# Kernel optimization log

Hardware: AMD Instinct MI355X
Metric: run time of the kernel (lower is better)

The kernel has to match this reference:

```python
import jax, jax.numpy as jnp
import numpy as np


def _mixture_log_cdf(x, pi, mu, s):
    # x: (B, C, H, W); pi/mu/s: (B, K, C, H, W); logistic log-CDF = log_sigmoid(z)
    z = (x[:, None] - mu) * jnp.exp(-s)
    return jax.scipy.special.logsumexp(
        jax.nn.log_softmax(pi, axis=1) + jax.nn.log_sigmoid(z), axis=1)


def _mixture_log_pdf(x, pi, mu, s):
    # logistic log-pdf: -z - log_scale - 2*softplus(-z), z = (x - mu) / exp(s)
    z = (x[:, None] - mu) * jnp.exp(-s)
    log_pdf = -z - s - 2.0 * jax.nn.softplus(-z)
    return jax.scipy.special.logsumexp(
        jax.nn.log_softmax(pi, axis=1) + log_pdf, axis=1)


def setup_inputs() -> dict:
    key = jax.random.key(0)
    B, C, H, W, K = 16, 64, 64, 64, 16
    Ch = C // 2
    ks = jax.random.split(key, 6)
    return {
        'x': jax.random.normal(ks[0], (B, C, H, W), jnp.float32),
        'sldj': jnp.zeros((B,), jnp.float32),
        'a': jax.random.normal(ks[1], (B, Ch, H, W), jnp.float32),
        'b': jax.random.normal(ks[2], (B, Ch, H, W), jnp.float32),
        'pi': jax.random.normal(ks[3], (B, K, Ch, H, W), jnp.float32),
        'mu': jax.random.normal(ks[4], (B, K, Ch, H, W), jnp.float32),
        's': jax.random.normal(ks[5], (B, K, Ch, H, W), jnp.float32),
    }


def reference(x, sldj, a, b, pi, mu, s):
    C = x.shape[1]
    x_change, x_id = x[:, :C // 2], x[:, C // 2:]
    # forward direction (reverse=False)
    log_cdf = _mixture_log_cdf(x_change, pi, mu, s)   # (B, C/2, H, W)
    u = jnp.exp(log_cdf)
    # logistic.inverse: logit(u); ldj = -log(u) - log(1-u)
    out = jnp.log(u) - jnp.log1p(-u)
    scale_ldj = -jnp.log(u) - jnp.log1p(-u)
    out = (out + b) * jnp.exp(a)
    logistic_ldj = _mixture_log_pdf(x_change, pi, mu, s)
    sldj = sldj + (logistic_ldj + scale_ldj + a).reshape(x.shape[0], -1).sum(-1)
    return jnp.concatenate([out, x_id], axis=1), sldj
```

## Files before the change

kernel.cpp:

```cpp
#include <hip/hip_runtime.h>
#include <math.h>

typedef float f32x4 __attribute__((ext_vector_type(4)));

constexpr int NB = 16, NK = 16, NCh = 32, NH = 64, NW = 64;
constexpr int HW = NH * NW;
constexpr int PER_BATCH = NCh * HW;
constexpr int NTOT = NB * PER_BATCH;
constexpr int PMS_BSTRIDE = NK * PER_BATCH;
constexpr int TILE = 1024;
constexpr int NTILES = NTOT / TILE;
constexpr int NBLOCKS = 1024;
constexpr int TPB = NTILES / NBLOCKS;

#define GLOAD4(dst, addr) \
    asm volatile("global_load_dwordx4 %0, %1, off" : "=v"(dst) : "v"(addr))

#define VMWAIT(N)                                              \
    do {                                                       \
        asm volatile("s_waitcnt vmcnt(" #N ")" ::: "memory");  \
        __builtin_amdgcn_sched_barrier(0);                     \
    } while (0)

#define ISSUE(buf, kbase)                                                     \
    do {                                                                      \
        _Pragma("unroll") for (int j = 0; j < 4; ++j) {                       \
            GLOAD4(Pb[buf][j], pp + (size_t)((kbase) + j) * PER_BATCH);       \
            GLOAD4(Mb[buf][j], mp + (size_t)((kbase) + j) * PER_BATCH);       \
            GLOAD4(Sb[buf][j], sp + (size_t)((kbase) + j) * PER_BATCH);       \
        }                                                                     \
    } while (0)

#define COMPUTE(buf)                                                          \
    do {                                                                      \
        _Pragma("unroll") for (int j = 0; j < 4; ++j) {                       \
            _Pragma("unroll") for (int e = 0; e < 4; ++e) {                   \
                const float es = __expf(-Sb[buf][j][e]);                      \
                float z = (x4[e] - Mb[buf][j][e]) * es;                       \
                z = fmaxf(z, -87.0f);                \
                const float t   = __expf(-z);                                 \
                const float sig = __builtin_amdgcn_rcpf(1.0f + t);            \
                const float ep  = __expf(Pb[buf][j][e]);                      \
                const float epc = ep * sig;                                   \
                const float cc  = epc * t;                                    \
                sumw[e]  += ep;                                               \
                scdf[e]  += epc;                                              \
                sccdf[e] += cc;                                               \
                spdf[e]   = fmaf(cc, sig * es, spdf[e]);                      \
            }                                                                 \
        }                                                                     \
    } while (0)

__launch_bounds__(256)
__global__ void mixlogcdf_kernel(const float* __restrict__ x,
                                 const float* __restrict__ a,
                                 const float* __restrict__ b,
                                 const float* __restrict__ pi,
                                 const float* __restrict__ mu,
                                 const float* __restrict__ s,
                                 float* __restrict__ out,
                                 float* __restrict__ ws) {
    const int blk = blockIdx.x;
    float srow = 0.f;

    for (int t = 0; t < TPB; ++t) {
        const int tile  = blk * TPB + t;
        const int gid   = tile * TILE + (threadIdx.x << 2);
        const int batch = gid >> 17;
        const int rem   = gid & (PER_BATCH - 1);
        const int xbase = (batch << 18) | rem;

        const size_t base = (size_t)batch * PMS_BSTRIDE + rem;
        const float* pp = pi + base;
        const float* mp = mu + base;
        const float* sp = s + base;

        f32x4 x4, a4, b4, id4;
        GLOAD4(x4, x + xbase);
        GLOAD4(a4, a + gid);
        GLOAD4(b4, b + gid);
        GLOAD4(id4, x + xbase + PER_BATCH);

        f32x4 Pb[2][4], Mb[2][4], Sb[2][4];
        ISSUE(0, 0);
        ISSUE(1, 4);

        float sumw[4]  = {0.f, 0.f, 0.f, 0.f};
        float scdf[4]  = {0.f, 0.f, 0.f, 0.f};
        float sccdf[4] = {0.f, 0.f, 0.f, 0.f};
        float spdf[4]  = {0.f, 0.f, 0.f, 0.f};

        VMWAIT(12);
        COMPUTE(0);
        ISSUE(0, 8);
        VMWAIT(12);
        COMPUTE(1);
        ISSUE(1, 12);
        VMWAIT(12);
        COMPUTE(0);
        VMWAIT(0);
        COMPUTE(1);

        f32x4 o4;
#pragma unroll
        for (int e = 0; e < 4; ++e) {
            const float lsp  = __logf(sumw[e]);
            const float lsc  = __logf(fmaxf(scdf[e], 1e-37f));
            const float lscc = __logf(fmaxf(sccdf[e], 1e-37f));
            const float lst  = __logf(fmaxf(spdf[e], 1e-37f));
            o4[e] = (lsc - lscc + b4[e]) * __expf(a4[e]);
            srow += lst + lsp - lsc - lscc + a4[e];
        }
        *(f32x4*)(out + xbase) = o4;
        *(f32x4*)(out + xbase + PER_BATCH) = id4;
    }

#pragma unroll
    for (int off = 32; off > 0; off >>= 1) srow += __shfl_down(srow, off, 64);
    __shared__ float wsum[4];
    const int lane = threadIdx.x & 63;
    const int wid  = threadIdx.x >> 6;
    if (lane == 0) wsum[wid] = srow;
    __syncthreads();
    if (threadIdx.x == 0) ws[blk] = wsum[0] + wsum[1] + wsum[2] + wsum[3];
}

__global__ void sldj_reduce_kernel(const float* __restrict__ sldj_in,
                                   const float* __restrict__ ws,
                                   float* __restrict__ out_sldj) {
    const int bb = blockIdx.x;
    float v = ws[bb * 64 + threadIdx.x];
#pragma unroll
    for (int off = 32; off > 0; off >>= 1) v += __shfl_down(v, off, 64);
    if (threadIdx.x == 0) out_sldj[bb] = sldj_in[bb] + v;
}

extern "C" void kernel_launch(void* const* d_in, const int* in_sizes, int n_in,
                              void* d_out, int out_size, void* d_ws, size_t ws_size,
                              hipStream_t stream) {
    const float* x    = (const float*)d_in[0];
    const float* sldj = (const float*)d_in[1];
    const float* a    = (const float*)d_in[2];
    const float* b    = (const float*)d_in[3];
    const float* pi   = (const float*)d_in[4];
    const float* mu   = (const float*)d_in[5];
    const float* s    = (const float*)d_in[6];

    float* out      = (float*)d_out;
    float* out_sldj = out + (size_t)NB * 2 * PER_BATCH;
    float* wsf      = (float*)d_ws;

    mixlogcdf_kernel<<<NBLOCKS, 256, 0, stream>>>(x, a, b, pi, mu, s, out, wsf);
    sldj_reduce_kernel<<<NB, 64, 0, stream>>>(sldj, wsf, out_sldj);
}
```

Baseline: 88.95 us.

## Stream pi and mu through LDS via global_load_lds double buffering

```diff
diff --git a/kernel.cpp b/kernel.cpp
--- a/kernel.cpp
+++ b/kernel.cpp
@@ -22,34 +22,16 @@
         __builtin_amdgcn_sched_barrier(0);                     \
     } while (0)
 
-#define ISSUE(buf, kbase)                                                     \
-    do {                                                                      \
-        _Pragma("unroll") for (int j = 0; j < 4; ++j) {                       \
-            GLOAD4(Pb[buf][j], pp + (size_t)((kbase) + j) * PER_BATCH);       \
-            GLOAD4(Mb[buf][j], mp + (size_t)((kbase) + j) * PER_BATCH);       \
-            GLOAD4(Sb[buf][j], sp + (size_t)((kbase) + j) * PER_BATCH);       \
-        }                                                                     \
+#define LGKM0()                                                \
+    do {                                                       \
+        asm volatile("s_waitcnt lgkmcnt(0)" ::: "memory");     \
+        __builtin_amdgcn_sched_barrier(0);                     \
     } while (0)
 
-#define COMPUTE(buf)                                                          \
-    do {                                                                      \
-        _Pragma("unroll") for (int j = 0; j < 4; ++j) {                       \
-            _Pragma("unroll") for (int e = 0; e < 4; ++e) {                   \
-                const float es = __expf(-Sb[buf][j][e]);                      \
-                float z = (x4[e] - Mb[buf][j][e]) * es;                       \
-                z = fmaxf(z, -87.0f);                \
-                const float t   = __expf(-z);                                 \
-                const float sig = __builtin_amdgcn_rcpf(1.0f + t);            \
-                const float ep  = __expf(Pb[buf][j][e]);                      \
-                const float epc = ep * sig;                                   \
-                const float cc  = epc * t;                                    \
-                sumw[e]  += ep;                                               \
-                scdf[e]  += epc;                                              \
-                sccdf[e] += cc;                                               \
-                spdf[e]   = fmaf(cc, sig * es, spdf[e]);                      \
-            }                                                                 \
-        }                                                                     \
-    } while (0)
+#define DMA16(gp, ldsptr)                                                     \
+    __builtin_amdgcn_global_load_lds(                                         \
+        (const __attribute__((address_space(1))) void*)(gp),                  \
+        (__attribute__((address_space(3))) void*)(ldsptr), 16, 0, 0)
 
 __launch_bounds__(256)
 __global__ void mixlogcdf_kernel(const float* __restrict__ x,
@@ -60,6 +42,11 @@
                                  const float* __restrict__ s,
                                  float* __restrict__ out,
                                  float* __restrict__ ws) {
+    __shared__ float lds[4 * 2048];
+    const int wid   = threadIdx.x >> 6;
+    const int lane  = threadIdx.x & 63;
+    const int wbase = wid * 2048;
+
     const int blk = blockIdx.x;
     float srow = 0.f;
 
@@ -70,10 +57,12 @@
         const int rem   = gid & (PER_BATCH - 1);
         const int xbase = (batch << 18) | rem;
 
-        const size_t base = (size_t)batch * PMS_BSTRIDE + rem;
-        const float* pp = pi + base;
-        const float* mp = mu + base;
-        const float* sp = s + base;
+        const size_t tbase = (size_t)batch * PMS_BSTRIDE + rem;
+        const float* sp = s + tbase;
+        const int wrem = (tile * TILE + wid * 256) & (PER_BATCH - 1);
+        const size_t wb = (size_t)batch * PMS_BSTRIDE + wrem + lane * 4;
+        const float* pw = pi + wb;
+        const float* mw = mu + wb;
 
         f32x4 x4, a4, b4, id4;
         GLOAD4(x4, x + xbase);
@@ -81,25 +70,73 @@
         GLOAD4(b4, b + gid);
         GLOAD4(id4, x + xbase + PER_BATCH);
 
-        f32x4 Pb[2][4], Mb[2][4], Sb[2][4];
-        ISSUE(0, 0);
-        ISSUE(1, 4);
+        f32x4 Sb[2][2];
+        DMA16(pw + 0 * PER_BATCH, &lds[wbase + 0 * 1024 + 0 * 512 + 0 * 256]);
+        DMA16(pw + 1 * PER_BATCH, &lds[wbase + 0 * 1024 + 1 * 512 + 0 * 256]);
+        DMA16(mw + 0 * PER_BATCH, &lds[wbase + 0 * 1024 + 0 * 512 + 1 * 256]);
+        DMA16(mw + 1 * PER_BATCH, &lds[wbase + 0 * 1024 + 1 * 512 + 1 * 256]);
+        GLOAD4(Sb[0][0], sp + 0 * PER_BATCH);
+        GLOAD4(Sb[0][1], sp + 1 * PER_BATCH);
+        DMA16(pw + 2 * PER_BATCH, &lds[wbase + 1 * 1024 + 0 * 512 + 0 * 256]);
+        DMA16(pw + 3 * PER_BATCH, &lds[wbase + 1 * 1024 + 1 * 512 + 0 * 256]);
+        DMA16(mw + 2 * PER_BATCH, &lds[wbase + 1 * 1024 + 0 * 512 + 1 * 256]);
+        DMA16(mw + 3 * PER_BATCH, &lds[wbase + 1 * 1024 + 1 * 512 + 1 * 256]);
+        GLOAD4(Sb[1][0], sp + 2 * PER_BATCH);
+        GLOAD4(Sb[1][1], sp + 3 * PER_BATCH);
 
         float sumw[4]  = {0.f, 0.f, 0.f, 0.f};
         float scdf[4]  = {0.f, 0.f, 0.f, 0.f};
         float sccdf[4] = {0.f, 0.f, 0.f, 0.f};
         float spdf[4]  = {0.f, 0.f, 0.f, 0.f};
 
-        VMWAIT(12);
-        COMPUTE(0);
-        ISSUE(0, 8);
-        VMWAIT(12);
-        COMPUTE(1);
-        ISSUE(1, 12);
-        VMWAIT(12);
-        COMPUTE(0);
-        VMWAIT(0);
-        COMPUTE(1);
+        VMWAIT(6);
+
+#pragma unroll
+        for (int c = 0; c < 8; ++c) {
+            const int buf = c & 1;
+            f32x4 Pv[2], Mv[2];
+            Pv[0] = *(const f32x4*)&lds[wbase + buf * 1024 + 0 * 512 + 0 * 256 + lane * 4];
+            Pv[1] = *(const f32x4*)&lds[wbase + buf * 1024 + 1 * 512 + 0 * 256 + lane * 4];
+            Mv[0] = *(const f32x4*)&lds[wbase + buf * 1024 + 0 * 512 + 1 * 256 + lane * 4];
+            Mv[1] = *(const f32x4*)&lds[wbase + buf * 1024 + 1 * 512 + 1 * 256 + lane * 4];
+            LGKM0();
+
+            if (c < 6) {
+                const int k0 = (c + 2) * 2;
+                DMA16(pw + (size_t)(k0 + 0) * PER_BATCH, &lds[wbase + buf * 1024 + 0 * 512 + 0 * 256]);
+                DMA16(pw + (size_t)(k0 + 1) * PER_BATCH, &lds[wbase + buf * 1024 + 1 * 512 + 0 * 256]);
+                DMA16(mw + (size_t)(k0 + 0) * PER_BATCH, &lds[wbase + buf * 1024 + 0 * 512 + 1 * 256]);
+                DMA16(mw + (size_t)(k0 + 1) * PER_BATCH, &lds[wbase + buf * 1024 + 1 * 512 + 1 * 256]);
+            }
+
+#pragma unroll
+            for (int kk = 0; kk < 2; ++kk) {
+#pragma unroll
+                for (int e = 0; e < 4; ++e) {
+                    const float es = __expf(-Sb[buf][kk][e]);
+                    float z = (x4[e] - Mv[kk][e]) * es;
+                    z = fmaxf(z, -87.0f);
+                    const float tt  = __expf(-z);
+                    const float sig = __builtin_amdgcn_rcpf(1.0f + tt);
+                    const float ep  = __expf(Pv[kk][e]);
+                    const float epc = ep * sig;
+                    const float cc  = epc * tt;
+                    sumw[e]  += ep;
+                    scdf[e]  += epc;
+                    sccdf[e] += cc;
+                    spdf[e]   = fmaf(cc, sig * es, spdf[e]);
+                }
+            }
+
+            if (c < 6) {
+                const int k0 = (c + 2) * 2;
+                GLOAD4(Sb[buf][0], sp + (size_t)(k0 + 0) * PER_BATCH);
+                GLOAD4(Sb[buf][1], sp + (size_t)(k0 + 1) * PER_BATCH);
+            }
+
+            if (c < 6)      VMWAIT(6);
+            else if (c == 6) VMWAIT(0);
+        }
 
         f32x4 o4;
 #pragma unroll
@@ -118,8 +155,6 @@
 #pragma unroll
     for (int off = 32; off > 0; off >>= 1) srow += __shfl_down(srow, off, 64);
     __shared__ float wsum[4];
-    const int lane = threadIdx.x & 63;
-    const int wid  = threadIdx.x >> 6;
     if (lane == 0) wsum[wid] = srow;
     __syncthreads();
     if (threadIdx.x == 0) ws[blk] = wsum[0] + wsum[1] + wsum[2] + wsum[3];
```

New measurement: 94.03 us. +5.7%, slower.
